# Performance work log

Hardware: AMD Instinct MI355X
Metric: run time of the kernel (lower is better)

The kernel has to match this reference:

```python
import jax, jax.numpy as jnp
import numpy as np

D_MODEL, D_FF, N_EXPERTS, TOP_K = 768, 3072, 8, 2
B, S = 2, 1024
LN_EPS = 1e-5


def setup_inputs() -> dict:
    key = jax.random.key(0)
    k1, k2, k3, k4 = jax.random.split(key, 4)
    return {
        "hidden_states": jax.random.normal(k1, (B, S, D_MODEL), dtype=jnp.float32),
        "ln_gamma": jnp.ones((D_MODEL,), dtype=jnp.float32),
        "ln_beta": jnp.zeros((D_MODEL,), dtype=jnp.float32),
        "router_w": jax.random.normal(k2, (D_MODEL, N_EXPERTS), dtype=jnp.float32) * 0.02,
        "w1": jax.random.normal(k3, (N_EXPERTS, D_MODEL, D_FF), dtype=jnp.float32) * 0.02,
        "w2": jax.random.normal(k4, (N_EXPERTS, D_FF, D_MODEL), dtype=jnp.float32) * 0.02,
    }


def _layernorm(x, gamma, beta):
    mu = jnp.mean(x, axis=-1, keepdims=True)
    var = jnp.mean(jnp.square(x - mu), axis=-1, keepdims=True)
    return (x - mu) * jax.lax.rsqrt(var + LN_EPS) * gamma + beta


def reference(hidden_states, ln_gamma, ln_beta, router_w, w1, w2):
    Bz, Sz, D = hidden_states.shape
    residual = hidden_states
    x = _layernorm(hidden_states, ln_gamma, ln_beta)
    tokens = x.reshape(-1, D)                       # [T, D]
    T = tokens.shape[0]

    # Router: softmax over experts, top-k selection, gate normalization
    logits = tokens @ router_w                      # [T, E]
    probs = jax.nn.softmax(logits, axis=-1)
    topw, topi = jax.lax.top_k(probs, TOP_K)        # [T, K]
    topw = topw / jnp.sum(topw, axis=-1, keepdims=True)  # normalize_gates=True

    # Dense gate matrix [T, E] (zero for unselected experts)
    gates = jnp.zeros((T, N_EXPERTS), dtype=tokens.dtype)
    gates = gates.at[jnp.arange(T)[:, None], topi].set(topw)

    # Per-expert FFN (silu, no bias), weighted combine
    h = jnp.einsum('td,edf->etf', tokens, w1)       # [E, T, F]
    h = jax.nn.silu(h)
    y = jnp.einsum('etf,efd->etd', h, w2)           # [E, T, D]
    out = jnp.einsum('te,etd->td', gates, y)        # [T, D]

    return residual + out.reshape(Bz, Sz, D)
```

## Files before the change

### kernel.cpp

```cpp
#include <hip/hip_runtime.h>
#include <hip/hip_bf16.h>
#include <math.h>

#define T_TOK 2048
#define DM 768
#define DF 3072
#define NE 8

typedef __attribute__((ext_vector_type(4))) float f32x4;
typedef __attribute__((ext_vector_type(8))) short bf16x8;

static __device__ __forceinline__ ushort f2bf(float f) {
    union { float f; unsigned u; } x; x.f = f;
    unsigned r = x.u + 0x7fff + ((x.u >> 16) & 1);
    return (ushort)(r >> 16);
}
static __device__ __forceinline__ float bf2f(ushort u) {
    union { unsigned u; float f; } x; x.u = ((unsigned)u) << 16; return x.f;
}
static __device__ __forceinline__ unsigned pk2(float lo, float hi) {
    return (unsigned)f2bf(lo) | ((unsigned)f2bf(hi) << 16);
}

__global__ __launch_bounds__(256) void ln_router_kernel(
    const float* __restrict__ hs, const float* __restrict__ gamma,
    const float* __restrict__ beta, const float* __restrict__ rw,
    ushort* __restrict__ xbf, float* __restrict__ topw, int* __restrict__ topi,
    int* __restrict__ counts)
{
    int t = blockIdx.x;
    int tid = threadIdx.x;
    const float* row = hs + (size_t)t * DM;
    float v[3];
    v[0] = row[tid]; v[1] = row[tid + 256]; v[2] = row[tid + 512];
    float s  = v[0] + v[1] + v[2];
    float sq = v[0]*v[0] + v[1]*v[1] + v[2]*v[2];
    #pragma unroll
    for (int off = 32; off > 0; off >>= 1) {
        s  += __shfl_down(s, off);
        sq += __shfl_down(sq, off);
    }
    __shared__ float wsum[4], wsq[4];
    __shared__ float pl[4][8];
    int lane = tid & 63, wv = tid >> 6;
    if (lane == 0) { wsum[wv] = s; wsq[wv] = sq; }
    __syncthreads();
    float tot  = wsum[0] + wsum[1] + wsum[2] + wsum[3];
    float totq = wsq[0] + wsq[1] + wsq[2] + wsq[3];
    float mu = tot * (1.0f / 768.0f);
    float var = totq * (1.0f / 768.0f) - mu * mu;
    float rstd = rsqrtf(var + 1e-5f);

    float p[8];
    #pragma unroll
    for (int e = 0; e < 8; e++) p[e] = 0.f;
    #pragma unroll
    for (int i = 0; i < 3; i++) {
        int d = tid + i * 256;
        float yv = (v[i] - mu) * rstd * gamma[d] + beta[d];
        xbf[(size_t)t * DM + d] = f2bf(yv);
        const float* r8 = rw + (size_t)d * 8;
        #pragma unroll
        for (int e = 0; e < 8; e++) p[e] += yv * r8[e];
    }
    #pragma unroll
    for (int off = 32; off > 0; off >>= 1) {
        #pragma unroll
        for (int e = 0; e < 8; e++) p[e] += __shfl_down(p[e], off);
    }
    if (lane == 0) {
        #pragma unroll
        for (int e = 0; e < 8; e++) pl[wv][e] = p[e];
    }
    __syncthreads();
    if (tid == 0) {
        float lg[8];
        #pragma unroll
        for (int e = 0; e < 8; e++) lg[e] = pl[0][e] + pl[1][e] + pl[2][e] + pl[3][e];
        int i0 = 0; float l0 = lg[0];
        #pragma unroll
        for (int e = 1; e < 8; e++) if (lg[e] > l0) { l0 = lg[e]; i0 = e; }
        int i1 = -1; float l1 = -3.4e38f;
        #pragma unroll
        for (int e = 0; e < 8; e++) if (e != i0 && lg[e] > l1) { l1 = lg[e]; i1 = e; }
        float w0 = 1.0f / (1.0f + __expf(l1 - l0));
        topi[2 * t] = i0;  topi[2 * t + 1] = i1;
        topw[2 * t] = w0;  topw[2 * t + 1] = 1.0f - w0;
        atomicAdd(&counts[i0], 1);
        atomicAdd(&counts[i1], 1);
    }
}

__global__ __launch_bounds__(256) void bucket_kernel(
    const int* __restrict__ topi, int* __restrict__ ctl,
    int* __restrict__ bucket_tok, int* __restrict__ tok_slot)
{
    int t = blockIdx.x * 256 + threadIdx.x;
    if (t >= T_TOK) return;
    int offs[8]; int acc = 0;
    #pragma unroll
    for (int e = 0; e < 8; e++) { offs[e] = acc; acc += ctl[e]; }
    #pragma unroll
    for (int k = 0; k < 2; k++) {
        int e = topi[2 * t + k];
        int pos = atomicAdd(&ctl[16 + e], 1);
        int idx = offs[e] + pos;
        bucket_tok[idx] = t;
        tok_slot[2 * t + k] = idx;
    }
}

template<bool SILU, bool GATHER, int NT, int SPLITS>
__global__ __launch_bounds__(256) void moe_gemm(
    const ushort* __restrict__ A, const float* __restrict__ W,
    ushort* __restrict__ C, const int* __restrict__ ctl,
    const int* __restrict__ bucket_tok, int K, int N)
{
    int bid = blockIdx.x;
    int e = bid & 7;
    int j = bid >> 3;
    int mt = j & 15;
    int c = j >> 4;
    int nt = c % NT;
    int sk = c / NT;
    int cnt = ctl[e];
    if (mt * 128 >= cnt) return;
    int off = 0;
    #pragma unroll
    for (int q = 0; q < 8; q++) if (q < e) off += ctl[q];
    const int Ks = K / SPLITS;
    int kbase = sk * Ks;

    __shared__ ushort Al[2][128 * 32];
    __shared__ unsigned Bl[2][16 * 128];

    int tid = threadIdx.x, lane = tid & 63, wv = tid >> 6;
    int kchunk = (lane & 3) * 8;

    const ushort* aptr[2];
    #pragma unroll
    for (int i = 0; i < 2; i++) {
        int r = i * 64 + wv * 16 + (lane >> 2);
        int gr = mt * 128 + r;
        if (gr >= cnt) gr = cnt - 1;
        if (GATHER) aptr[i] = A + (size_t)bucket_tok[off + gr] * K;
        else        aptr[i] = A + (size_t)(off + gr) * K;
    }

    const float* Wb = W + (size_t)e * ((size_t)K * N);
    int n0 = nt * 128;
    int rp_[2], cc_[2];
    #pragma unroll
    for (int ii = 0; ii < 2; ii++) {
        int item = wv * 128 + ii * 64 + lane;
        rp_[ii] = item >> 5;
        cc_[ii] = item & 31;
    }

    f32x4 acc[4][4];
    #pragma unroll
    for (int m = 0; m < 4; m++)
        #pragma unroll
        for (int n = 0; n < 4; n++)
            acc[m][n] = (f32x4){0.f, 0.f, 0.f, 0.f};

    int wr = wv >> 1, wc = wv & 1;
    int l15 = lane & 15, kq = lane >> 4;
    int ldstA = (wv * 16) * 32 + lane * 8;
    int xk = (kq & 1) << 4;

    float4 breg[2][2];

    auto stageA = [&](int buf, int k0) {
        #pragma unroll
        for (int i = 0; i < 2; i++) {
            __builtin_amdgcn_global_load_lds(
                (const __attribute__((address_space(1))) void*)(aptr[i] + k0 + kchunk),
                (__attribute__((address_space(3))) void*)(&Al[buf][i * 64 * 32 + ldstA]),
                16, 0, 0);
        }
    };
    auto bload = [&](int k0) {
        #pragma unroll
        for (int ii = 0; ii < 2; ii++) {
            const float* s = Wb + (size_t)(k0 + 2 * rp_[ii]) * N + n0 + 4 * cc_[ii];
            breg[ii][0] = *(const float4*)s;
            breg[ii][1] = *(const float4*)(s + N);
        }
    };
    auto bwrite = [&](int buf) {
        #pragma unroll
        for (int ii = 0; ii < 2; ii++) {
            uint4 r;
            r.x = pk2(breg[ii][0].x, breg[ii][1].x);
            r.y = pk2(breg[ii][0].y, breg[ii][1].y);
            r.z = pk2(breg[ii][0].z, breg[ii][1].z);
            r.w = pk2(breg[ii][0].w, breg[ii][1].w);
            *(uint4*)&Bl[buf][rp_[ii] * 128 + ((4 * cc_[ii]) ^ ((rp_[ii] & 7) << 2))] = r;
        }
    };

    const int nk = Ks >> 5;
    stageA(0, kbase);
    bload(kbase);
    asm volatile("s_waitcnt vmcnt(0)" ::: "memory");
    bwrite(0);
    asm volatile("s_waitcnt lgkmcnt(0)" ::: "memory");
    __builtin_amdgcn_s_barrier();

    for (int ks = 0; ks < nk; ks++) {
        int cur = ks & 1;
        bool more = (ks + 1 < nk);
        if (more) {
            stageA(cur ^ 1, kbase + (ks + 1) * 32);
            bload(kbase + (ks + 1) * 32);
        }
        bf16x8 af[4], bfr[4];
        #pragma unroll
        for (int m = 0; m < 4; m++)
            af[m] = *(const bf16x8*)&Al[cur][(wr * 64 + m * 16 + l15) * 32 + kq * 8];
        const unsigned* Blc = &Bl[cur][0];
        #pragma unroll
        for (int n = 0; n < 4; n++) {
            int ncol = wc * 64 + n * 16 + l15;
            union { uint4 u; bf16x8 h; } cvu;
            cvu.u.x = Blc[(kq * 4 + 0) * 128 + (ncol ^ (xk | 0))];
            cvu.u.y = Blc[(kq * 4 + 1) * 128 + (ncol ^ (xk | 4))];
            cvu.u.z = Blc[(kq * 4 + 2) * 128 + (ncol ^ (xk | 8))];
            cvu.u.w = Blc[(kq * 4 + 3) * 128 + (ncol ^ (xk | 12))];
            bfr[n] = cvu.h;
        }
        __builtin_amdgcn_s_setprio(1);
        #pragma unroll
        for (int m = 0; m < 4; m++)
            #pragma unroll
            for (int n = 0; n < 4; n++)
                acc[m][n] = __builtin_amdgcn_mfma_f32_16x16x32_bf16(af[m], bfr[n], acc[m][n], 0, 0, 0);
        __builtin_amdgcn_s_setprio(0);
        if (more) {
            asm volatile("s_waitcnt vmcnt(0)" ::: "memory");
            bwrite(cur ^ 1);
        }
        asm volatile("s_waitcnt vmcnt(0) lgkmcnt(0)" ::: "memory");
        __builtin_amdgcn_s_barrier();
    }

    #pragma unroll
    for (int m = 0; m < 4; m++) {
        #pragma unroll
        for (int n = 0; n < 4; n++) {
            #pragma unroll
            for (int jj = 0; jj < 4; jj++) {
                int gr = mt * 128 + wr * 64 + m * 16 + kq * 4 + jj;
                if (gr < cnt) {
                    float v = acc[m][n][jj];
                    if (SILU) v = v / (1.0f + __expf(-v));
                    int col = nt * 128 + wc * 64 + n * 16 + l15;
                    C[((size_t)sk * (T_TOK * 2) + off + gr) * N + col] = f2bf(v);
                }
            }
        }
    }
}

template<int SPLITS>
__global__ __launch_bounds__(256) void combine_kernel(
    const float* __restrict__ hs, const ushort* __restrict__ Yp,
    const float* __restrict__ topw, const int* __restrict__ tok_slot,
    float* __restrict__ out)
{
    int t = blockIdx.x, tid = threadIdx.x;
    int s0 = tok_slot[2 * t], s1 = tok_slot[2 * t + 1];
    float w0 = topw[2 * t], w1 = topw[2 * t + 1];
    const float* h = hs + (size_t)t * DM;
    float* o = out + (size_t)t * DM;
    #pragma unroll
    for (int i = 0; i < 3; i++) {
        int d = tid + i * 256;
        float y0 = 0.f, y1 = 0.f;
        #pragma unroll
        for (int s = 0; s < SPLITS; s++) {
            y0 += bf2f(Yp[((size_t)s * (T_TOK * 2) + s0) * DM + d]);
            y1 += bf2f(Yp[((size_t)s * (T_TOK * 2) + s1) * DM + d]);
        }
        o[d] = h[d] + w0 * y0 + w1 * y1;
    }
}

extern "C" void kernel_launch(void* const* d_in, const int* in_sizes, int n_in,
                              void* d_out, int out_size, void* d_ws, size_t ws_size,
                              hipStream_t stream)
{
    const float* hs    = (const float*)d_in[0];
    const float* gamma = (const float*)d_in[1];
    const float* beta  = (const float*)d_in[2];
    const float* rw    = (const float*)d_in[3];
    const float* w1    = (const float*)d_in[4];
    const float* w2    = (const float*)d_in[5];
    float* out = (float*)d_out;
    char* ws = (char*)d_ws;

    size_t o = 0;
    auto alc = [&](size_t b) { size_t r = o; o += (b + 255) & ~255ULL; return r; };
    int*      ctl        = (int*)(ws + alc(256));
    float*    topw       = (float*)(ws + alc((size_t)T_TOK * 2 * 4));
    int*      topi       = (int*)(ws + alc((size_t)T_TOK * 2 * 4));
    int*      tok_slot   = (int*)(ws + alc((size_t)T_TOK * 2 * 4));
    int*      bucket_tok = (int*)(ws + alc((size_t)T_TOK * 2 * 4));
    ushort*   xbf        = (ushort*)(ws + alc((size_t)T_TOK * DM * 2));
    ushort*   Hg         = (ushort*)(ws + alc((size_t)T_TOK * 2 * DF * 2));
    size_t yp_off        = alc((size_t)4 * T_TOK * 2 * DM * 2);
    ushort*   Yp         = (ushort*)(ws + yp_off);
    bool can_split       = (o <= ws_size);

    hipMemsetAsync(ctl, 0, 256, stream);
    ln_router_kernel<<<T_TOK, 256, 0, stream>>>(hs, gamma, beta, rw, xbf, topw, topi, ctl);
    bucket_kernel<<<8, 256, 0, stream>>>(topi, ctl, bucket_tok, tok_slot);

    moe_gemm<true, true, 24, 1><<<8 * 16 * 24, 256, 0, stream>>>(
        xbf, w1, Hg, ctl, bucket_tok, DM, DF);

    if (can_split) {
        moe_gemm<false, false, 6, 4><<<8 * 16 * 6 * 4, 256, 0, stream>>>(
            Hg, w2, Yp, ctl, bucket_tok, DF, DM);
        combine_kernel<4><<<T_TOK, 256, 0, stream>>>(hs, Yp, topw, tok_slot, out);
    } else {
        moe_gemm<false, false, 6, 1><<<8 * 16 * 6, 256, 0, stream>>>(
            Hg, w2, Yp, ctl, bucket_tok, DF, DM);
        combine_kernel<1><<<T_TOK, 256, 0, stream>>>(hs, Yp, topw, tok_slot, out);
    }
}
```

Baseline: 212.3 us.

## Triple-buffer MoE GEMM tiles with two-deep prefetch and swizzled A layout

Moves the expert GEMM from double to triple LDS buffering, with two alternating register sets for the fp32 weight loads so global loads run two k-steps ahead. Partial vmcnt waits replace full drains, so one stage's loads stay in flight during compute. The A tile also gets an XOR swizzle on its k-chunk position to reduce LDS bank conflicts on fragment reads. The cost is more LDS and registers, which may lower occupancy. The loop is unrolled by two and assumes nk is even.

```diff
diff --git a/kernel.cpp b/kernel.cpp
--- a/kernel.cpp
+++ b/kernel.cpp
@@ -129,13 +129,13 @@
     #pragma unroll
     for (int q = 0; q < 8; q++) if (q < e) off += ctl[q];
     const int Ks = K / SPLITS;
-    int kbase = sk * Ks;
-
-    __shared__ ushort Al[2][128 * 32];
-    __shared__ unsigned Bl[2][16 * 128];
+    const int kbase = sk * Ks;
+
+    __shared__ ushort Al[3][128 * 32];
+    __shared__ unsigned Bl[3][16 * 128];
 
     int tid = threadIdx.x, lane = tid & 63, wv = tid >> 6;
-    int kchunk = (lane & 3) * 8;
+    int kchA = ((lane & 3) ^ ((lane >> 3) & 3)) * 8;
 
     const ushort* aptr[2];
     #pragma unroll
@@ -169,56 +169,41 @@
     int ldstA = (wv * 16) * 32 + lane * 8;
     int xk = (kq & 1) << 4;
 
-    float4 breg[2][2];
-
     auto stageA = [&](int buf, int k0) {
         #pragma unroll
         for (int i = 0; i < 2; i++) {
             __builtin_amdgcn_global_load_lds(
-                (const __attribute__((address_space(1))) void*)(aptr[i] + k0 + kchunk),
+                (const __attribute__((address_space(1))) void*)(aptr[i] + k0 + kchA),
                 (__attribute__((address_space(3))) void*)(&Al[buf][i * 64 * 32 + ldstA]),
                 16, 0, 0);
         }
     };
-    auto bload = [&](int k0) {
+    auto bload = [&](float4 (&br)[2][2], int k0) {
         #pragma unroll
         for (int ii = 0; ii < 2; ii++) {
             const float* s = Wb + (size_t)(k0 + 2 * rp_[ii]) * N + n0 + 4 * cc_[ii];
-            breg[ii][0] = *(const float4*)s;
-            breg[ii][1] = *(const float4*)(s + N);
+            br[ii][0] = *(const float4*)s;
+            br[ii][1] = *(const float4*)(s + N);
         }
     };
-    auto bwrite = [&](int buf) {
+    auto bwrite = [&](float4 (&br)[2][2], int buf) {
         #pragma unroll
         for (int ii = 0; ii < 2; ii++) {
             uint4 r;
-            r.x = pk2(breg[ii][0].x, breg[ii][1].x);
-            r.y = pk2(breg[ii][0].y, breg[ii][1].y);
-            r.z = pk2(breg[ii][0].z, breg[ii][1].z);
-            r.w = pk2(breg[ii][0].w, breg[ii][1].w);
+            r.x = pk2(br[ii][0].x, br[ii][1].x);
+            r.y = pk2(br[ii][0].y, br[ii][1].y);
+            r.z = pk2(br[ii][0].z, br[ii][1].z);
+            r.w = pk2(br[ii][0].w, br[ii][1].w);
             *(uint4*)&Bl[buf][rp_[ii] * 128 + ((4 * cc_[ii]) ^ ((rp_[ii] & 7) << 2))] = r;
         }
     };
-
-    const int nk = Ks >> 5;
-    stageA(0, kbase);
-    bload(kbase);
-    asm volatile("s_waitcnt vmcnt(0)" ::: "memory");
-    bwrite(0);
-    asm volatile("s_waitcnt lgkmcnt(0)" ::: "memory");
-    __builtin_amdgcn_s_barrier();
-
-    for (int ks = 0; ks < nk; ks++) {
-        int cur = ks & 1;
-        bool more = (ks + 1 < nk);
-        if (more) {
-            stageA(cur ^ 1, kbase + (ks + 1) * 32);
-            bload(kbase + (ks + 1) * 32);
-        }
+    auto compute = [&](int cur) {
         bf16x8 af[4], bfr[4];
         #pragma unroll
-        for (int m = 0; m < 4; m++)
-            af[m] = *(const bf16x8*)&Al[cur][(wr * 64 + m * 16 + l15) * 32 + kq * 8];
+        for (int m = 0; m < 4; m++) {
+            int row = wr * 64 + m * 16 + l15;
+            af[m] = *(const bf16x8*)&Al[cur][row * 32 + ((kq ^ ((row >> 1) & 3)) << 3)];
+        }
         const unsigned* Blc = &Bl[cur][0];
         #pragma unroll
         for (int n = 0; n < 4; n++) {
@@ -237,13 +222,44 @@
             for (int n = 0; n < 4; n++)
                 acc[m][n] = __builtin_amdgcn_mfma_f32_16x16x32_bf16(af[m], bfr[n], acc[m][n], 0, 0, 0);
         __builtin_amdgcn_s_setprio(0);
-        if (more) {
-            asm volatile("s_waitcnt vmcnt(0)" ::: "memory");
-            bwrite(cur ^ 1);
-        }
-        asm volatile("s_waitcnt vmcnt(0) lgkmcnt(0)" ::: "memory");
-        __builtin_amdgcn_s_barrier();
-    }
+    };
+
+    #define FENCE asm volatile("" ::: "memory")
+    float4 brg0[2][2], brg1[2][2];
+    const int nk = Ks >> 5;
+
+    bload(brg0, kbase); FENCE;
+    stageA(0, kbase); FENCE;
+    bload(brg1, kbase + 32); FENCE;
+    stageA(1, kbase + 32); FENCE;
+    bwrite(brg0, 0);
+    asm volatile("s_waitcnt vmcnt(6)" ::: "memory");
+    asm volatile("s_waitcnt lgkmcnt(0)" ::: "memory");
+    __builtin_amdgcn_s_barrier();
+
+    #define BODY(T, BLD, BWR) { \
+        int t_ = (T); \
+        bool more2 = (t_ + 2 < nk); \
+        if (more2) { \
+            bload(BLD, kbase + (t_ + 2) * 32); FENCE; \
+            stageA((t_ + 2) % 3, kbase + (t_ + 2) * 32); FENCE; \
+        } \
+        compute(t_ % 3); \
+        if (t_ + 1 < nk) { \
+            bwrite(BWR, (t_ + 1) % 3); \
+            if (more2) asm volatile("s_waitcnt vmcnt(6)" ::: "memory"); \
+            else       asm volatile("s_waitcnt vmcnt(0)" ::: "memory"); \
+            asm volatile("s_waitcnt lgkmcnt(0)" ::: "memory"); \
+            __builtin_amdgcn_s_barrier(); \
+        } \
+    }
+
+    for (int t = 0; t < nk; t += 2) {
+        BODY(t, brg0, brg1);
+        BODY(t + 1, brg1, brg0);
+    }
+    #undef BODY
+    #undef FENCE
 
     #pragma unroll
     for (int m = 0; m < 4; m++) {
```

Result: slower. 395.0 us (+86.1%).

## Schedule MoE GEMM over compact tile list, swizzle A LDS, use packed bf16 convert

Applied to the files above, without the earlier changes.

Adds a scan kernel that builds a compact list of (expert, row offset, row count) tiles, so the GEMM grid covers only real tiles (at most 40) instead of 8x16 mostly-empty expert/m-tile slots that exit early. It also XOR-swizzles the A tile's K-chunk placement in LDS to reduce bank conflicts on fragment reads, and replaces the software float-to-bf16 rounding for B with the v_cvt_pk_bf16_f32 instruction. This adds a single-thread serial kernel launch, and NTILES_MAX=40 assumes the total tile count never exceeds 40. With 4096 routed rows spread over 8 experts, up to 39 tiles are possible, so the bound holds.

```diff
diff --git a/kernel.cpp b/kernel.cpp
--- a/kernel.cpp
+++ b/kernel.cpp
@@ -6,6 +6,7 @@
 #define DM 768
 #define DF 3072
 #define NE 8
+#define NTILES_MAX 40
 
 typedef __attribute__((ext_vector_type(4))) float f32x4;
 typedef __attribute__((ext_vector_type(8))) short bf16x8;
@@ -19,7 +20,9 @@
     union { unsigned u; float f; } x; x.u = ((unsigned)u) << 16; return x.f;
 }
 static __device__ __forceinline__ unsigned pk2(float lo, float hi) {
-    return (unsigned)f2bf(lo) | ((unsigned)f2bf(hi) << 16);
+    unsigned r;
+    asm("v_cvt_pk_bf16_f32 %0, %1, %2" : "=v"(r) : "v"(lo), "v"(hi));
+    return r;
 }
 
 __global__ __launch_bounds__(256) void ln_router_kernel(
@@ -91,6 +94,22 @@
     }
 }
 
+__global__ void scan_kernel(int* __restrict__ ctl, int4* __restrict__ tiles)
+{
+    if (threadIdx.x == 0 && blockIdx.x == 0) {
+        int acc = 0, nt = 0;
+        for (int e = 0; e < 8; e++) {
+            int cnt = ctl[e];
+            for (int m0 = 0; m0 < cnt; m0 += 128) {
+                tiles[nt] = make_int4(e, acc + m0, min(128, cnt - m0), 0);
+                nt++;
+            }
+            acc += cnt;
+        }
+        ctl[24] = nt;
+    }
+}
+
 __global__ __launch_bounds__(256) void bucket_kernel(
     const int* __restrict__ topi, int* __restrict__ ctl,
     int* __restrict__ bucket_tok, int* __restrict__ tok_slot)
@@ -114,37 +133,33 @@
 __global__ __launch_bounds__(256) void moe_gemm(
     const ushort* __restrict__ A, const float* __restrict__ W,
     ushort* __restrict__ C, const int* __restrict__ ctl,
-    const int* __restrict__ bucket_tok, int K, int N)
+    const int* __restrict__ bucket_tok, const int4* __restrict__ tiles,
+    int K, int N)
 {
     int bid = blockIdx.x;
-    int e = bid & 7;
-    int j = bid >> 3;
-    int mt = j & 15;
-    int c = j >> 4;
+    int c  = bid % (NT * SPLITS);
+    int tl = bid / (NT * SPLITS);
+    if (tl >= ctl[24]) return;
     int nt = c % NT;
     int sk = c / NT;
-    int cnt = ctl[e];
-    if (mt * 128 >= cnt) return;
-    int off = 0;
-    #pragma unroll
-    for (int q = 0; q < 8; q++) if (q < e) off += ctl[q];
+    int4 t4 = tiles[tl];
+    int e = t4.x, grow0 = t4.y, rows = t4.z;
     const int Ks = K / SPLITS;
-    int kbase = sk * Ks;
+    const int kbase = sk * Ks;
 
     __shared__ ushort Al[2][128 * 32];
     __shared__ unsigned Bl[2][16 * 128];
 
     int tid = threadIdx.x, lane = tid & 63, wv = tid >> 6;
-    int kchunk = (lane & 3) * 8;
+    int kchA = ((lane & 3) ^ ((lane >> 3) & 3)) * 8;
 
     const ushort* aptr[2];
     #pragma unroll
     for (int i = 0; i < 2; i++) {
         int r = i * 64 + wv * 16 + (lane >> 2);
-        int gr = mt * 128 + r;
-        if (gr >= cnt) gr = cnt - 1;
-        if (GATHER) aptr[i] = A + (size_t)bucket_tok[off + gr] * K;
-        else        aptr[i] = A + (size_t)(off + gr) * K;
+        int rr = r < rows ? r : rows - 1;
+        if (GATHER) aptr[i] = A + (size_t)bucket_tok[grow0 + rr] * K;
+        else        aptr[i] = A + (size_t)(grow0 + rr) * K;
     }
 
     const float* Wb = W + (size_t)e * ((size_t)K * N);
@@ -169,13 +184,13 @@
     int ldstA = (wv * 16) * 32 + lane * 8;
     int xk = (kq & 1) << 4;
 
-    float4 breg[2][2];
+    float4 brg[2][2];
 
     auto stageA = [&](int buf, int k0) {
         #pragma unroll
         for (int i = 0; i < 2; i++) {
             __builtin_amdgcn_global_load_lds(
-                (const __attribute__((address_space(1))) void*)(aptr[i] + k0 + kchunk),
+                (const __attribute__((address_space(1))) void*)(aptr[i] + k0 + kchA),
                 (__attribute__((address_space(3))) void*)(&Al[buf][i * 64 * 32 + ldstA]),
                 16, 0, 0);
         }
@@ -184,41 +199,28 @@
         #pragma unroll
         for (int ii = 0; ii < 2; ii++) {
             const float* s = Wb + (size_t)(k0 + 2 * rp_[ii]) * N + n0 + 4 * cc_[ii];
-            breg[ii][0] = *(const float4*)s;
-            breg[ii][1] = *(const float4*)(s + N);
+            brg[ii][0] = *(const float4*)s;
+            brg[ii][1] = *(const float4*)(s + N);
         }
     };
     auto bwrite = [&](int buf) {
         #pragma unroll
         for (int ii = 0; ii < 2; ii++) {
             uint4 r;
-            r.x = pk2(breg[ii][0].x, breg[ii][1].x);
-            r.y = pk2(breg[ii][0].y, breg[ii][1].y);
-            r.z = pk2(breg[ii][0].z, breg[ii][1].z);
-            r.w = pk2(breg[ii][0].w, breg[ii][1].w);
+            r.x = pk2(brg[ii][0].x, brg[ii][1].x);
+            r.y = pk2(brg[ii][0].y, brg[ii][1].y);
+            r.z = pk2(brg[ii][0].z, brg[ii][1].z);
+            r.w = pk2(brg[ii][0].w, brg[ii][1].w);
             *(uint4*)&Bl[buf][rp_[ii] * 128 + ((4 * cc_[ii]) ^ ((rp_[ii] & 7) << 2))] = r;
         }
     };
-
-    const int nk = Ks >> 5;
-    stageA(0, kbase);
-    bload(kbase);
-    asm volatile("s_waitcnt vmcnt(0)" ::: "memory");
-    bwrite(0);
-    asm volatile("s_waitcnt lgkmcnt(0)" ::: "memory");
-    __builtin_amdgcn_s_barrier();
-
-    for (int ks = 0; ks < nk; ks++) {
-        int cur = ks & 1;
-        bool more = (ks + 1 < nk);
-        if (more) {
-            stageA(cur ^ 1, kbase + (ks + 1) * 32);
-            bload(kbase + (ks + 1) * 32);
-        }
+    auto compute = [&](int cur) {
         bf16x8 af[4], bfr[4];
         #pragma unroll
-        for (int m = 0; m < 4; m++)
-            af[m] = *(const bf16x8*)&Al[cur][(wr * 64 + m * 16 + l15) * 32 + kq * 8];
+        for (int m = 0; m < 4; m++) {
+            int row = wr * 64 + m * 16 + l15;
+            af[m] = *(const bf16x8*)&Al[cur][row * 32 + ((kq ^ ((row >> 1) & 3)) << 3)];
+        }
         const unsigned* Blc = &Bl[cur][0];
         #pragma unroll
         for (int n = 0; n < 4; n++) {
@@ -237,6 +239,24 @@
             for (int n = 0; n < 4; n++)
                 acc[m][n] = __builtin_amdgcn_mfma_f32_16x16x32_bf16(af[m], bfr[n], acc[m][n], 0, 0, 0);
         __builtin_amdgcn_s_setprio(0);
+    };
+
+    const int nk = Ks >> 5;
+    stageA(0, kbase);
+    bload(kbase);
+    asm volatile("s_waitcnt vmcnt(0)" ::: "memory");
+    bwrite(0);
+    asm volatile("s_waitcnt lgkmcnt(0)" ::: "memory");
+    __builtin_amdgcn_s_barrier();
+
+    for (int ks = 0; ks < nk; ks++) {
+        int cur = ks & 1;
+        bool more = (ks + 1 < nk);
+        if (more) {
+            stageA(cur ^ 1, kbase + (ks + 1) * 32);
+            bload(kbase + (ks + 1) * 32);
+        }
+        compute(cur);
         if (more) {
             asm volatile("s_waitcnt vmcnt(0)" ::: "memory");
             bwrite(cur ^ 1);
@@ -251,12 +271,12 @@
         for (int n = 0; n < 4; n++) {
             #pragma unroll
             for (int jj = 0; jj < 4; jj++) {
-                int gr = mt * 128 + wr * 64 + m * 16 + kq * 4 + jj;
-                if (gr < cnt) {
+                int r = wr * 64 + m * 16 + kq * 4 + jj;
+                if (r < rows) {
                     float v = acc[m][n][jj];
                     if (SILU) v = v / (1.0f + __expf(-v));
                     int col = nt * 128 + wc * 64 + n * 16 + l15;
-                    C[((size_t)sk * (T_TOK * 2) + off + gr) * N + col] = f2bf(v);
+                    C[((size_t)sk * (T_TOK * 2) + grow0 + r) * N + col] = f2bf(v);
                 }
             }
         }
@@ -303,6 +323,7 @@
     size_t o = 0;
     auto alc = [&](size_t b) { size_t r = o; o += (b + 255) & ~255ULL; return r; };
     int*      ctl        = (int*)(ws + alc(256));
+    int4*     tiles      = (int4*)(ws + alc(NTILES_MAX * 16));
     float*    topw       = (float*)(ws + alc((size_t)T_TOK * 2 * 4));
     int*      topi       = (int*)(ws + alc((size_t)T_TOK * 2 * 4));
     int*      tok_slot   = (int*)(ws + alc((size_t)T_TOK * 2 * 4));
@@ -315,18 +336,19 @@
 
     hipMemsetAsync(ctl, 0, 256, stream);
     ln_router_kernel<<<T_TOK, 256, 0, stream>>>(hs, gamma, beta, rw, xbf, topw, topi, ctl);
+    scan_kernel<<<1, 64, 0, stream>>>(ctl, tiles);
     bucket_kernel<<<8, 256, 0, stream>>>(topi, ctl, bucket_tok, tok_slot);
 
-    moe_gemm<true, true, 24, 1><<<8 * 16 * 24, 256, 0, stream>>>(
-        xbf, w1, Hg, ctl, bucket_tok, DM, DF);
+    moe_gemm<true, true, 24, 1><<<NTILES_MAX * 24, 256, 0, stream>>>(
+        xbf, w1, Hg, ctl, bucket_tok, tiles, DM, DF);
 
     if (can_split) {
-        moe_gemm<false, false, 6, 4><<<8 * 16 * 6 * 4, 256, 0, stream>>>(
-            Hg, w2, Yp, ctl, bucket_tok, DF, DM);
+        moe_gemm<false, false, 6, 4><<<NTILES_MAX * 6 * 4, 256, 0, stream>>>(
+            Hg, w2, Yp, ctl, bucket_tok, tiles, DF, DM);
         combine_kernel<4><<<T_TOK, 256, 0, stream>>>(hs, Yp, topw, tok_slot, out);
     } else {
-        moe_gemm<false, false, 6, 1><<<8 * 16 * 6, 256, 0, stream>>>(
-            Hg, w2, Yp, ctl, bucket_tok, DF, DM);
+        moe_gemm<false, false, 6, 1><<<NTILES_MAX * 6, 256, 0, stream>>>(
+            Hg, w2, Yp, ctl, bucket_tok, tiles, DF, DM);
         combine_kernel<1><<<T_TOK, 256, 0, stream>>>(hs, Yp, topw, tok_slot, out);
     }
 }
```

Result: no change. 214.3 us (+0.9%).
